# Kernel optimization log

Measured on AMD Instinct MI355X. Metric: run time of the kernel, lower is better.

## Reference

```python
import jax, jax.numpy as jnp
import numpy as np

N_QUBITS = 12
DIM = 2 ** N_QUBITS  # 4096

_H = (jnp.array([[1.0, 1.0], [1.0, -1.0]]) / np.sqrt(2.0)).astype(jnp.complex64)
_X = jnp.array([[0.0, 1.0], [1.0, 0.0]], dtype=jnp.complex64)


def setup_inputs() -> dict:
    key = jax.random.key(0)
    k1, k2 = jax.random.split(key)
    state = jax.random.normal(k1, (8, 512, DIM), dtype=jnp.float32)
    params = jax.random.normal(k2, (N_QUBITS,), dtype=jnp.float32)
    return {"state": state, "params": params}


def _to_quantum(x):
    # faithful to _classical_to_quantum_inspired: normalize, phase = acos(|v|), sign * exp(i*phase)
    norms = jnp.linalg.norm(x, axis=-1, keepdims=True)
    v = x / (norms + 1e-8)
    mag = jnp.minimum(jnp.abs(v), 1.0)
    q = (jnp.sign(v) * jnp.exp(1j * jnp.arccos(mag))).astype(jnp.complex64)
    nrm = jnp.sqrt(jnp.sum(q.real ** 2 + q.imag ** 2, axis=-1, keepdims=True))
    return q / nrm.astype(jnp.complex64)


def _axis(q):
    # qubit q = bit q (LSB); tensor axes ordered MSB-first after batch axis 0
    return 1 + (N_QUBITS - 1 - q)


def _apply_1q(full, q, U):
    ax = _axis(q)
    moved = jnp.moveaxis(full, ax, -1)
    out = jnp.einsum('...b,ab->...a', moved, U)
    return jnp.moveaxis(out, -1, ax)


def _apply_ctrl(full, c, t, U):
    # apply U on target qubit t where control qubit c == 1
    axc = _axis(c)
    b0 = jnp.take(full, 0, axis=axc)
    b1 = jnp.take(full, 1, axis=axc)
    axt = _axis(t)
    axt_sub = axt - 1 if axt > axc else axt
    moved = jnp.moveaxis(b1, axt_sub, -1)
    b1n = jnp.moveaxis(jnp.einsum('...b,ab->...a', moved, U), -1, axt_sub)
    return jnp.stack([b0, b1n], axis=axc)


def _rx(theta):
    c = jnp.cos(theta / 2).astype(jnp.complex64)
    s = (-1j * jnp.sin(theta / 2)).astype(jnp.complex64)
    return jnp.stack([jnp.stack([c, s]), jnp.stack([s, c])])


def reference(state, params):
    B, T, D = state.shape
    psi = _to_quantum(state.reshape(B * T, D))  # (N, 2**n) complex64
    full = psi.reshape((B * T,) + (2,) * N_QUBITS)
    for q in range(N_QUBITS):
        full = _apply_1q(full, q, _H)                                  # Hadamard
        full = _apply_ctrl(full, q, (q + 1) % N_QUBITS, _rx(params[q]))  # controlled-RX
        if q < N_QUBITS - 1:
            full = _apply_ctrl(full, q, q + 1, _X)                     # CNOT
    amp = full.reshape(B * T, D)
    probs = amp.real ** 2 + amp.imag ** 2  # measurement probabilities
    return probs.reshape(B, T, D).astype(jnp.float32)
```

## Files before the change

kernel.cpp:

```cpp
#include <hip/hip_runtime.h>

#define NQ  12
#define DIM 4096
#define TPB 256

__device__ __forceinline__ float wave_reduce(float v) {
#pragma unroll
    for (int m = 32; m >= 1; m >>= 1) v += __shfl_xor(v, m, 64);
    return v;
}

template <int MC, int MT, bool XGATE>
__device__ __forceinline__ void apply_layer(float2* a, float ct, float sn) {
    const float h = 0.70710678118654752440f;
#pragma unroll
    for (int i = 0; i < 16; ++i) {
        if (i & MC) continue;
        const int j = i | MC;
        const float2 t0 = a[i], t1 = a[j];
        a[i] = make_float2(h * (t0.x + t1.x), h * (t0.y + t1.y));
        a[j] = make_float2(h * (t0.x - t1.x), h * (t0.y - t1.y));
    }
#pragma unroll
    for (int i = 0; i < 16; ++i) {
        if (!(i & MC) || (i & MT)) continue;
        const int j = i | MT;
        const float2 b0 = a[i], b1 = a[j];
        const float s0x = sn * b0.y, s0y = -sn * b0.x;
        const float s1x = sn * b1.y, s1y = -sn * b1.x;
        if (XGATE) {
            a[i] = make_float2(fmaf(ct, b1.x, s0x), fmaf(ct, b1.y, s0y));
            a[j] = make_float2(fmaf(ct, b0.x, s1x), fmaf(ct, b0.y, s1y));
        } else {
            a[i] = make_float2(fmaf(ct, b0.x, s1x), fmaf(ct, b0.y, s1y));
            a[j] = make_float2(fmaf(ct, b1.x, s0x), fmaf(ct, b1.y, s0y));
        }
    }
}

__global__ __launch_bounds__(TPB) void qlayer_kernel(
        const float* __restrict__ state, const float* __restrict__ params,
        float* __restrict__ out) {
    __shared__ float2 amp[DIM];
    __shared__ float red1[4], red2[4];
    __shared__ float cth[NQ], sth[NQ];

    const int t = threadIdx.x;
    const long long sbase = (long long)blockIdx.x * DIM;

    if (t < NQ) {
        const float th = params[t] * 0.5f;
        cth[t] = cosf(th);
        sth[t] = sinf(th);
    }

    float x[16];
    const float4* gp = (const float4*)(state + sbase + t * 16);
#pragma unroll
    for (int j = 0; j < 4; ++j) {
        const float4 v = gp[j];
        x[4 * j + 0] = v.x; x[4 * j + 1] = v.y;
        x[4 * j + 2] = v.z; x[4 * j + 3] = v.w;
    }
    float ss = 0.f;
#pragma unroll
    for (int k = 0; k < 16; ++k) ss = fmaf(x[k], x[k], ss);
    ss = wave_reduce(ss);
    const int wid = t >> 6;
    if ((t & 63) == 0) red1[wid] = ss;
    __syncthreads();
    const float nrm  = sqrtf(red1[0] + red1[1] + red1[2] + red1[3]);
    const float invd = 1.0f / (nrm + 1e-8f);

    float2 a[16];
    float n2 = 0.f;
#pragma unroll
    for (int k = 0; k < 16; ++k) {
        const float v   = x[k] * invd;
        const float mag = fminf(fabsf(v), 1.0f);
        const float sgn = (v > 0.f) ? 1.f : ((v < 0.f) ? -1.f : 0.f);
        const float re  = sgn * mag;
        const float im  = sgn * sqrtf(fmaxf(1.0f - mag * mag, 0.f));
        a[k] = make_float2(re, im);
        n2 += re * re + im * im;
    }
    n2 = wave_reduce(n2);
    if ((t & 63) == 0) red2[wid] = n2;
    __syncthreads();
    const float inv2 = 1.0f / (red2[0] + red2[1] + red2[2] + red2[3]);

    apply_layer<1, 2, true>(a, cth[0], sth[0]);
    apply_layer<2, 4, true>(a, cth[1], sth[1]);
    apply_layer<4, 8, true>(a, cth[2], sth[2]);
#pragma unroll
    for (int r = 0; r < 16; ++r) amp[t * 16 + r] = a[r];
    __syncthreads();

    {
        const int base = (t & 7) | ((t >> 3) << 7);
#pragma unroll
        for (int r = 0; r < 16; ++r) a[r] = amp[base | (r << 3)];
        apply_layer<1, 2, true>(a, cth[3], sth[3]);
        apply_layer<2, 4, true>(a, cth[4], sth[4]);
        apply_layer<4, 8, true>(a, cth[5], sth[5]);
#pragma unroll
        for (int r = 0; r < 16; ++r) amp[base | (r << 3)] = a[r];
    }
    __syncthreads();

    {
        const int base = (t & 63) | ((t >> 6) << 10);
#pragma unroll
        for (int r = 0; r < 16; ++r) a[r] = amp[base | (r << 6)];
        apply_layer<1, 2, true>(a, cth[6], sth[6]);
        apply_layer<2, 4, true>(a, cth[7], sth[7]);
        apply_layer<4, 8, true>(a, cth[8], sth[8]);
#pragma unroll
        for (int r = 0; r < 16; ++r) amp[base | (r << 6)] = a[r];
    }
    __syncthreads();

    {
        const int base = t << 1;
#pragma unroll
        for (int r = 0; r < 16; ++r)
            a[r] = amp[base | ((r & 7) << 9) | (r >> 3)];
        apply_layer<1, 2, true >(a, cth[9],  sth[9]);
        apply_layer<2, 4, true >(a, cth[10], sth[10]);
        apply_layer<4, 8, false>(a, cth[11], sth[11]);

        float2* outp = (float2*)(out + sbase);
#pragma unroll
        for (int r = 0; r < 8; ++r) {
            const int idx = base | ((r & 7) << 9);
            const float p0 = (a[r].x * a[r].x + a[r].y * a[r].y) * inv2;
            const float p1 = (a[r | 8].x * a[r | 8].x + a[r | 8].y * a[r | 8].y) * inv2;
            outp[idx >> 1] = make_float2(p0, p1);
        }
    }
}

extern "C" void kernel_launch(void* const* d_in, const int* in_sizes, int n_in,
                              void* d_out, int out_size, void* d_ws, size_t ws_size,
                              hipStream_t stream) {
    (void)in_sizes; (void)n_in; (void)out_size; (void)d_ws; (void)ws_size;
    const float* state  = (const float*)d_in[0];
    const float* params = (const float*)d_in[1];
    float* out = (float*)d_out;
    qlayer_kernel<<<dim3(4096), dim3(TPB), 0, stream>>>(state, params, out);
}
```

Before: 133.4 us.

## Drop second norm reduction, fold Hadamard scaling, swizzle split LDS, broadcast params

Removes the second block-wide reduction by relying on each amplitude having unit modulus, so the total is the dimension. The 1/sqrt2 factors of all twelve Hadamards are folded together with that normalization into one constant output scale. Shared memory becomes separate real/imag arrays with an XOR swizzle to cut bank conflicts on the strided exchanges. Gate cos/sin values are broadcast via readlane instead of shared memory. The fixed scale is wrong for exact-zero inputs, and the unscaled intermediates grow in magnitude.

```diff
diff --git a/kernel.cpp b/kernel.cpp
--- a/kernel.cpp
+++ b/kernel.cpp
@@ -3,6 +3,8 @@
 #define NQ  12
 #define DIM 4096
 #define TPB 256
+
+__device__ __forceinline__ int SW(int i) { return i ^ ((i >> 5) & 31); }
 
 __device__ __forceinline__ float wave_reduce(float v) {
 #pragma unroll
@@ -10,16 +12,17 @@
     return v;
 }
 
+#define BCAST(v, q) __uint_as_float(__builtin_amdgcn_readlane(__float_as_uint(v), (q)))
+
 template <int MC, int MT, bool XGATE>
 __device__ __forceinline__ void apply_layer(float2* a, float ct, float sn) {
-    const float h = 0.70710678118654752440f;
 #pragma unroll
     for (int i = 0; i < 16; ++i) {
         if (i & MC) continue;
         const int j = i | MC;
         const float2 t0 = a[i], t1 = a[j];
-        a[i] = make_float2(h * (t0.x + t1.x), h * (t0.y + t1.y));
-        a[j] = make_float2(h * (t0.x - t1.x), h * (t0.y - t1.y));
+        a[i] = make_float2(t0.x + t1.x, t0.y + t1.y);
+        a[j] = make_float2(t0.x - t1.x, t0.y - t1.y);
     }
 #pragma unroll
     for (int i = 0; i < 16; ++i) {
@@ -41,100 +44,109 @@
 __global__ __launch_bounds__(TPB) void qlayer_kernel(
         const float* __restrict__ state, const float* __restrict__ params,
         float* __restrict__ out) {
-    __shared__ float2 amp[DIM];
-    __shared__ float red1[4], red2[4];
-    __shared__ float cth[NQ], sth[NQ];
+    __shared__ float sre[DIM];
+    __shared__ float sim[DIM];
 
     const int t = threadIdx.x;
+    const int lane = t & 63;
     const long long sbase = (long long)blockIdx.x * DIM;
 
-    if (t < NQ) {
-        const float th = params[t] * 0.5f;
-        cth[t] = cosf(th);
-        sth[t] = sinf(th);
-    }
+    const float th = params[lane < NQ ? lane : 0] * 0.5f;
+    const float cl = cosf(th);
+    const float sl = sinf(th);
 
     float x[16];
     const float4* gp = (const float4*)(state + sbase + t * 16);
+    float ss = 0.f;
 #pragma unroll
     for (int j = 0; j < 4; ++j) {
         const float4 v = gp[j];
         x[4 * j + 0] = v.x; x[4 * j + 1] = v.y;
         x[4 * j + 2] = v.z; x[4 * j + 3] = v.w;
+        ss = fmaf(v.x, v.x, ss); ss = fmaf(v.y, v.y, ss);
+        ss = fmaf(v.z, v.z, ss); ss = fmaf(v.w, v.w, ss);
     }
-    float ss = 0.f;
-#pragma unroll
-    for (int k = 0; k < 16; ++k) ss = fmaf(x[k], x[k], ss);
     ss = wave_reduce(ss);
-    const int wid = t >> 6;
-    if ((t & 63) == 0) red1[wid] = ss;
+    if (lane == 0) sre[t >> 6] = ss;
     __syncthreads();
-    const float nrm  = sqrtf(red1[0] + red1[1] + red1[2] + red1[3]);
+    const float nrm  = sqrtf(sre[0] + sre[1] + sre[2] + sre[3]);
     const float invd = 1.0f / (nrm + 1e-8f);
+    __syncthreads();
 
     float2 a[16];
-    float n2 = 0.f;
 #pragma unroll
     for (int k = 0; k < 16; ++k) {
         const float v   = x[k] * invd;
-        const float mag = fminf(fabsf(v), 1.0f);
-        const float sgn = (v > 0.f) ? 1.f : ((v < 0.f) ? -1.f : 0.f);
-        const float re  = sgn * mag;
-        const float im  = sgn * sqrtf(fmaxf(1.0f - mag * mag, 0.f));
+        const float re  = fminf(fmaxf(v, -1.0f), 1.0f);
+        const float imb = sqrtf(fmaxf(1.0f - re * re, 0.f));
+        const float im  = (v > 0.f) ? imb : ((v < 0.f) ? -imb : 0.f);
         a[k] = make_float2(re, im);
-        n2 += re * re + im * im;
     }
-    n2 = wave_reduce(n2);
-    if ((t & 63) == 0) red2[wid] = n2;
-    __syncthreads();
-    const float inv2 = 1.0f / (red2[0] + red2[1] + red2[2] + red2[3]);
 
-    apply_layer<1, 2, true>(a, cth[0], sth[0]);
-    apply_layer<2, 4, true>(a, cth[1], sth[1]);
-    apply_layer<4, 8, true>(a, cth[2], sth[2]);
+    apply_layer<1, 2, true>(a, BCAST(cl, 0), BCAST(sl, 0));
+    apply_layer<2, 4, true>(a, BCAST(cl, 1), BCAST(sl, 1));
+    apply_layer<4, 8, true>(a, BCAST(cl, 2), BCAST(sl, 2));
 #pragma unroll
-    for (int r = 0; r < 16; ++r) amp[t * 16 + r] = a[r];
+    for (int r = 0; r < 16; ++r) {
+        const int s = SW(t * 16 + r);
+        sre[s] = a[r].x; sim[s] = a[r].y;
+    }
     __syncthreads();
 
     {
         const int base = (t & 7) | ((t >> 3) << 7);
 #pragma unroll
-        for (int r = 0; r < 16; ++r) a[r] = amp[base | (r << 3)];
-        apply_layer<1, 2, true>(a, cth[3], sth[3]);
-        apply_layer<2, 4, true>(a, cth[4], sth[4]);
-        apply_layer<4, 8, true>(a, cth[5], sth[5]);
+        for (int r = 0; r < 16; ++r) {
+            const int s = SW(base | (r << 3));
+            a[r] = make_float2(sre[s], sim[s]);
+        }
+        apply_layer<1, 2, true>(a, BCAST(cl, 3), BCAST(sl, 3));
+        apply_layer<2, 4, true>(a, BCAST(cl, 4), BCAST(sl, 4));
+        apply_layer<4, 8, true>(a, BCAST(cl, 5), BCAST(sl, 5));
 #pragma unroll
-        for (int r = 0; r < 16; ++r) amp[base | (r << 3)] = a[r];
+        for (int r = 0; r < 16; ++r) {
+            const int s = SW(base | (r << 3));
+            sre[s] = a[r].x; sim[s] = a[r].y;
+        }
     }
     __syncthreads();
 
     {
         const int base = (t & 63) | ((t >> 6) << 10);
 #pragma unroll
-        for (int r = 0; r < 16; ++r) a[r] = amp[base | (r << 6)];
-        apply_layer<1, 2, true>(a, cth[6], sth[6]);
-        apply_layer<2, 4, true>(a, cth[7], sth[7]);
-        apply_layer<4, 8, true>(a, cth[8], sth[8]);
+        for (int r = 0; r < 16; ++r) {
+            const int s = SW(base | (r << 6));
+            a[r] = make_float2(sre[s], sim[s]);
+        }
+        apply_layer<1, 2, true>(a, BCAST(cl, 6), BCAST(sl, 6));
+        apply_layer<2, 4, true>(a, BCAST(cl, 7), BCAST(sl, 7));
+        apply_layer<4, 8, true>(a, BCAST(cl, 8), BCAST(sl, 8));
 #pragma unroll
-        for (int r = 0; r < 16; ++r) amp[base | (r << 6)] = a[r];
+        for (int r = 0; r < 16; ++r) {
+            const int s = SW(base | (r << 6));
+            sre[s] = a[r].x; sim[s] = a[r].y;
+        }
     }
     __syncthreads();
 
     {
         const int base = t << 1;
 #pragma unroll
-        for (int r = 0; r < 16; ++r)
-            a[r] = amp[base | ((r & 7) << 9) | (r >> 3)];
-        apply_layer<1, 2, true >(a, cth[9],  sth[9]);
-        apply_layer<2, 4, true >(a, cth[10], sth[10]);
-        apply_layer<4, 8, false>(a, cth[11], sth[11]);
+        for (int r = 0; r < 16; ++r) {
+            const int s = SW(base | ((r & 7) << 9) | (r >> 3));
+            a[r] = make_float2(sre[s], sim[s]);
+        }
+        apply_layer<1, 2, true >(a, BCAST(cl, 9),  BCAST(sl, 9));
+        apply_layer<2, 4, true >(a, BCAST(cl, 10), BCAST(sl, 10));
+        apply_layer<4, 8, false>(a, BCAST(cl, 11), BCAST(sl, 11));
 
+        const float scale = 0x1p-24f;
         float2* outp = (float2*)(out + sbase);
 #pragma unroll
         for (int r = 0; r < 8; ++r) {
             const int idx = base | ((r & 7) << 9);
-            const float p0 = (a[r].x * a[r].x + a[r].y * a[r].y) * inv2;
-            const float p1 = (a[r | 8].x * a[r | 8].x + a[r | 8].y * a[r | 8].y) * inv2;
+            const float p0 = (a[r].x * a[r].x + a[r].y * a[r].y) * scale;
+            const float p1 = (a[r | 8].x * a[r | 8].x + a[r | 8].y * a[r | 8].y) * scale;
             outp[idx >> 1] = make_float2(p0, p1);
         }
     }
```

Measured after the change: 128.7 us. 3.5% less time.
